# Optimization experiments

Hardware: AMD Instinct MI355X
Metric: run time of the kernel (lower is better)

The kernel has to match this reference:

```python
import jax, jax.numpy as jnp
from jax import lax
import numpy as np

SHAPE = (50, 60, 65)   # -> after net: (17, 27, 32), flatten = 14688
NEG = 0.01             # LeakyReLU default slope
B, N = 8, 80000        # batch size, total active voxels


def _lrelu(x):
    return jnp.where(x >= 0, x, NEG * x)


def _sparse_conv(x, w, b, m):
    # Regular (non-submanifold) sparse conv == dense VALID conv on densified
    # input (inactive sites are 0 so they contribute nothing). Output site is
    # active iff any input site in the kernel footprint is active; bias is
    # added only at active output sites.
    k = w.shape[2]
    y = lax.conv_general_dilated(x, w, (1, 1, 1), 'VALID',
                                 dimension_numbers=('NCDHW', 'OIDHW', 'NCDHW'))
    m2 = lax.reduce_window(m, 0.0, lax.max, (1, 1, k, k, k), (1, 1, 1, 1, 1), 'VALID')
    y = jnp.where(m2 > 0, y + b[None, :, None, None, None], 0.0)
    return y, m2


def _sparse_maxpool(x, m, k):
    # spconv SparseMaxPool: max over ACTIVE sites only (inactive excluded, not 0)
    xm = jnp.where(m > 0, x, -jnp.inf)
    p = lax.reduce_window(xm, -jnp.inf, lax.max, (1, 1, k, k, k), (1, 1, 1, 1, 1), 'VALID')
    m2 = lax.reduce_window(m, 0.0, lax.max, (1, 1, k, k, k), (1, 1, 1, 1, 1), 'VALID')
    return jnp.where(m2 > 0, p, 0.0), m2


def setup_inputs() -> dict:
    key = jax.random.key(0)
    ks = jax.random.split(key, 24)
    D, H, W = SHAPE
    features = jax.random.normal(ks[0], (N, 1), dtype=jnp.float32)
    bi = jax.random.randint(ks[1], (N,), 0, B)
    zi = jax.random.randint(ks[2], (N,), 0, D)
    yi = jax.random.randint(ks[3], (N,), 0, H)
    xi = jax.random.randint(ks[4], (N,), 0, W)
    coors = jnp.stack([bi, zi, yi, xi], axis=1).astype(jnp.int32)
    s = 0.05
    p = {}
    p['w1'] = jax.random.normal(ks[5], (32, 1, 4, 4, 4), jnp.float32) * s
    p['b1'] = jax.random.normal(ks[6], (32,), jnp.float32) * s
    p['w2'] = jax.random.normal(ks[7], (32, 32, 4, 4, 4), jnp.float32) * s
    p['b2'] = jax.random.normal(ks[8], (32,), jnp.float32) * s
    p['w3'] = jax.random.normal(ks[9], (32, 32, 4, 4, 4), jnp.float32) * s
    p['b3'] = jax.random.normal(ks[10], (32,), jnp.float32) * s
    p['w4'] = jax.random.normal(ks[11], (32, 32, 4, 4, 4), jnp.float32) * s
    p['b4'] = jax.random.normal(ks[12], (32,), jnp.float32) * s
    p['w5'] = jax.random.normal(ks[13], (32, 32, 4, 4, 4), jnp.float32) * s
    p['b5'] = jax.random.normal(ks[14], (32,), jnp.float32) * s
    p['w6'] = jax.random.normal(ks[15], (32, 32, 4, 4, 4), jnp.float32) * s
    p['b6'] = jax.random.normal(ks[16], (32,), jnp.float32) * s
    p['w7'] = jax.random.normal(ks[17], (1, 32, 4, 4, 4), jnp.float32) * s
    p['b7'] = jax.random.normal(ks[18], (1,), jnp.float32) * s
    p['W8'] = jax.random.normal(ks[19], (14688, 1000), jnp.float32) * 0.01
    p['b8'] = jax.random.normal(ks[20], (1000,), jnp.float32) * s
    p['W9'] = jax.random.normal(ks[21], (1000, 1000), jnp.float32) * 0.03
    p['b9'] = jax.random.normal(ks[22], (1000,), jnp.float32) * s
    p['W10'] = jax.random.normal(ks[23], (1000, 1), jnp.float32) * 0.03
    p['b10'] = jnp.zeros((1,), jnp.float32)
    return dict(features=features, coors=coors, batch_size=B, **p)


def reference(features, coors, batch_size,
              w1, b1, w2, b2, w3, b3, w4, b4, w5, b5, w6, b6, w7, b7,
              W8, b8, W9, b9, W10, b10):
    D, H, W = SHAPE
    bi, zi, yi, xi = coors[:, 0], coors[:, 1], coors[:, 2], coors[:, 3]
    dense = jnp.zeros((batch_size, 1, D, H, W), features.dtype)
    dense = dense.at[bi, 0, zi, yi, xi].set(features[:, 0])
    mask = jnp.zeros((batch_size, 1, D, H, W), features.dtype)
    mask = mask.at[bi, 0, zi, yi, xi].set(1.0)

    x, m = _sparse_conv(dense, w1, b1, mask); x = _lrelu(x)
    x, m = _sparse_conv(x, w2, b2, m);        x = _lrelu(x)
    x, m = _sparse_maxpool(x, m, 5)
    x, m = _sparse_conv(x, w3, b3, m);        x = _lrelu(x)
    x, m = _sparse_conv(x, w4, b4, m);        x = _lrelu(x)
    x, m = _sparse_maxpool(x, m, 5)
    x, m = _sparse_conv(x, w5, b5, m);        x = _lrelu(x)
    x, m = _sparse_conv(x, w6, b6, m);        x = _lrelu(x)
    x, m = _sparse_conv(x, w7, b7, m);        x = _lrelu(x)
    x, m = _sparse_maxpool(x, m, 5)

    # ToDense (inactive sites already 0) + Flatten -> [B, 14688]
    h = x.reshape(x.shape[0], -1)
    h = _lrelu(h @ W8 + b8)
    h = _lrelu(h @ W9 + b9)
    out = _lrelu(h @ W10 + b10)
    return out
```

## Files before the change

### kernel.cpp

```cpp
#include <hip/hip_runtime.h>
#include <cstddef>


#define NEGSLOPE 0.01f
#define NINF (-3.0e38f)

#define TZ 4
#define TY 4
#define TXT 16
#define IZ 7
#define IY 7
#define IX 19
#define NV (IZ*IY*IX)

typedef __attribute__((ext_vector_type(8)))  short    short8;
typedef __attribute__((ext_vector_type(4)))  unsigned uint4v;
typedef __attribute__((ext_vector_type(16))) float    floatx16;

__device__ __forceinline__ float lrelu(float v) { return v >= 0.f ? v : NEGSLOPE * v; }

__device__ __forceinline__ unsigned short f2bf(float f) {
  unsigned b = __float_as_uint(f);
  return (unsigned short)((b + 0x7fffu + ((b >> 16) & 1u)) >> 16);
}
__device__ __forceinline__ float bf2f(unsigned short h) {
  return __uint_as_float(((unsigned)h) << 16);
}
__device__ __forceinline__ unsigned splitpair(float a, float b, unsigned& lo) {
  unsigned short ha = f2bf(a), hb = f2bf(b);
  unsigned short la = f2bf(a - bf2f(ha)), lb = f2bf(b - bf2f(hb));
  lo = (unsigned)la | ((unsigned)lb << 16);
  return (unsigned)ha | ((unsigned)hb << 16);
}

__device__ __forceinline__ short8 ld_frag(const uint2* s2, int v, int oct) {
  uint2 u0 = s2[v * 5 + oct * 2];
  uint2 u1 = s2[v * 5 + oct * 2 + 1];
  uint4v t; t.x = u0.x; t.y = u0.y; t.z = u1.x; t.w = u1.y;
  return __builtin_bit_cast(short8, t);
}

__global__ void k_claim(const int* __restrict__ coors, unsigned* __restrict__ claim, int N) {
  int i = blockIdx.x * blockDim.x + threadIdx.x;
  if (i >= N) return;
  int b = coors[4*i], z = coors[4*i+1], y = coors[4*i+2], x = coors[4*i+3];
  int v = ((b*50 + z)*60 + y)*65 + x;
  atomicMax(&claim[v], (unsigned)(i + 1));
}

__global__ void k_scatter(const int* __restrict__ coors, const float* __restrict__ feat,
                          const unsigned* __restrict__ claim,
                          float* __restrict__ x0, float* __restrict__ m0, int N) {
  int i = blockIdx.x * blockDim.x + threadIdx.x;
  if (i >= N) return;
  int b = coors[4*i], z = coors[4*i+1], y = coors[4*i+2], x = coors[4*i+3];
  int v = ((b*50 + z)*60 + y)*65 + x;
  m0[v] = 1.f;
  if (claim[v] == (unsigned)(i + 1)) x0[v] = feat[i];
}

__global__ void k_repack(const float* __restrict__ w, float* __restrict__ wr, int CI, int CO) {
  int i = blockIdx.x * blockDim.x + threadIdx.x;
  int tot = CO * CI * 64;
  if (i >= tot) return;
  int k = i & 63;
  int ci = (i >> 6) % CI;
  int co = i / (64 * CI);
  wr[(k * CI + ci) * CO + co] = w[i];
}

__global__ void k_repack_mfma(const float* __restrict__ w, unsigned short* __restrict__ tbl) {
  int i = blockIdx.x * blockDim.x + threadIdx.x;
  if (i >= 64*4*2*64) return;
  int lane = i & 63; int t = i >> 6;
  int pack = t & 1; t >>= 1;
  int pass = t & 3; int tap = t >> 2;
  int co = lane & 31; int oct = lane >> 5;
#pragma unroll
  for (int j = 0; j < 8; ++j) {
    int k = oct * 8 + j;
    int ci = pass * 8 + (k & 7);
    int part = ((k >> 3) ^ pack) & 1;
    float wv = w[((co * 32 + ci) << 6) + tap];
    unsigned short wh = f2bf(wv);
    unsigned short r = part ? f2bf(wv - bf2f(wh)) : wh;
    tbl[(size_t)i * 8 + j] = r;
  }
}

__global__ void kd_z(const float* __restrict__ in, float* __restrict__ o,
                     int Zi, int Yi, int Xi, int Zo, int K, int nI) {
  int gid = blockIdx.x * blockDim.x + threadIdx.x;
  int perOut = Zo * Yi * Xi;
  if (gid >= nI * perOut) return;
  int item = gid / perOut;
  int r = gid - item * perOut;
  int x = r % Xi; int t = r / Xi;
  int y = t % Yi; int z = t / Yi;
  const float* ib = in + (size_t)item * Zi * Yi * Xi;
  float mx = 0.f;
  for (int d = 0; d < K; d++) mx = fmaxf(mx, ib[((z + d) * Yi + y) * Xi + x]);
  o[gid] = mx;
}

__global__ void kd_y(const float* __restrict__ in, float* __restrict__ o,
                     int Zo, int Yi, int Xi, int Yo, int K, int nI) {
  int gid = blockIdx.x * blockDim.x + threadIdx.x;
  int perOut = Zo * Yo * Xi;
  if (gid >= nI * perOut) return;
  int item = gid / perOut;
  int r = gid - item * perOut;
  int x = r % Xi; int t = r / Xi;
  int y = t % Yo; int z = t / Yo;
  const float* ib = in + (size_t)item * Zo * Yi * Xi;
  float mx = 0.f;
  for (int d = 0; d < K; d++) mx = fmaxf(mx, ib[(z * Yi + y + d) * Xi + x]);
  o[gid] = mx;
}

__global__ void kd_x(const float* __restrict__ in, float* __restrict__ o,
                     int Zo, int Yo, int Xi, int Xo, int K, int nI) {
  int gid = blockIdx.x * blockDim.x + threadIdx.x;
  int perOut = Zo * Yo * Xo;
  if (gid >= nI * perOut) return;
  int item = gid / perOut;
  int r = gid - item * perOut;
  int x = r % Xo; int t = r / Xo;
  int y = t % Yo; int z = t / Yo;
  const float* ib = in + (size_t)item * Zo * Yo * Xi;
  float mx = 0.f;
  for (int d = 0; d < K; d++) mx = fmaxf(mx, ib[(z * Yo + y) * Xi + x + d]);
  o[gid] = mx;
}

__global__ __launch_bounds__(256, 4)
void k_conv32m(const float* __restrict__ in, const unsigned short* __restrict__ tbl,
               const float* __restrict__ bias, const float* __restrict__ mo,
               float* __restrict__ out, int splitOut,
               int Zi, int Yi, int Xi, int Zo, int Yo, int Xo,
               int tilesZ, int tilesY, int tilesX) {
  __shared__ unsigned sU[NV * 10];
  const int perIn = Zi * Yi * Xi;
  const int perOut = Zo * Yo * Xo;
  int bid = blockIdx.x;
  int txi = bid % tilesX; bid /= tilesX;
  int tyi = bid % tilesY; bid /= tilesY;
  int tzi = bid % tilesZ; int item = bid / tilesZ;
  const int z0 = tzi * TZ, y0 = tyi * TY, x0 = txi * TXT;
  const int tid = threadIdx.x;
  const int lane = tid & 63;
  const int col = lane & 31;
  const int oct = lane >> 5;
  const int wv  = tid >> 6;

  int lvBase0, lvBase1;
  {
    int vt0 = (2*wv + 0)*32 + col;
    int vt1 = (2*wv + 1)*32 + col;
    lvBase0 = ((vt0 >> 6)*IY + ((vt0 >> 4) & 3))*IX + (vt0 & 15);
    lvBase1 = ((vt1 >> 6)*IY + ((vt1 >> 4) & 3))*IX + (vt1 & 15);
  }

  floatx16 acc0, acc1;
#pragma unroll
  for (int r = 0; r < 16; ++r) { acc0[r] = 0.f; acc1[r] = 0.f; }

  const char* inB = (const char*)in + (size_t)item * perIn * 128;
  const char* tb = (const char*)tbl + lane * 16;
  uint2* s2 = (uint2*)sU;

  const char* gptr[4];
  int lidx[4];
#pragma unroll
  for (int it = 0; it < 4; ++it) {
    int idx = tid + it * 256;
    gptr[it] = nullptr; lidx[it] = -1;
    if (idx < NV) {
      int iz = idx / (IY * IX); int r = idx - iz * (IY * IX);
      int iy = r / IX; int ix = r - iy * IX;
      int gz = z0 + iz, gy = y0 + iy, gx = x0 + ix;
      lidx[it] = idx * 5;
      if (gz < Zi && gy < Yi && gx < Xi)
        gptr[it] = inB + (size_t)((gz * Yi + gy) * Xi + gx) * 128;
    }
  }

  uint4 hreg[4], lreg[4];
  const uint4 zz = make_uint4(0u, 0u, 0u, 0u);
#pragma unroll
  for (int it = 0; it < 4; ++it) {
    hreg[it] = zz; lreg[it] = zz;
    if (gptr[it]) {
      hreg[it] = *(const uint4*)(gptr[it]);
      lreg[it] = *(const uint4*)(gptr[it] + 16);
    }
  }

#pragma unroll 1
  for (int p = 0; p < 4; ++p) {
    __syncthreads();
#pragma unroll
    for (int it = 0; it < 4; ++it) {
      if (lidx[it] >= 0) {
        s2[lidx[it] + 0] = make_uint2(hreg[it].x, hreg[it].y);
        s2[lidx[it] + 1] = make_uint2(hreg[it].z, hreg[it].w);
        s2[lidx[it] + 2] = make_uint2(lreg[it].x, lreg[it].y);
        s2[lidx[it] + 3] = make_uint2(lreg[it].z, lreg[it].w);
      }
    }
    __syncthreads();
    if (p < 3) {
      int po = (p + 1) * 32;
#pragma unroll
      for (int it = 0; it < 4; ++it) {
        hreg[it] = zz; lreg[it] = zz;
        if (gptr[it]) {
          hreg[it] = *(const uint4*)(gptr[it] + po);
          lreg[it] = *(const uint4*)(gptr[it] + po + 16);
        }
      }
    }

    const char* tp = tb + (size_t)p * 2048;
#pragma unroll 2
    for (int tap = 0; tap < 64; ++tap) {
      int kz = tap >> 4, ky = (tap >> 2) & 3, kx = tap & 3;
      int sOff = (kz * IY + ky) * IX + kx;
      short8 b0 = *(const short8*)(tp + (size_t)tap * 8192);
      short8 b1 = *(const short8*)(tp + (size_t)tap * 8192 + 1024);
      short8 a0 = ld_frag(s2, lvBase0 + sOff, oct);
      short8 a1 = ld_frag(s2, lvBase1 + sOff, oct);
      acc0 = __builtin_amdgcn_mfma_f32_32x32x16_bf16(a0, b0, acc0, 0, 0, 0);
      acc0 = __builtin_amdgcn_mfma_f32_32x32x16_bf16(a0, b1, acc0, 0, 0, 0);
      acc1 = __builtin_amdgcn_mfma_f32_32x32x16_bf16(a1, b0, acc1, 0, 0, 0);
      acc1 = __builtin_amdgcn_mfma_f32_32x32x16_bf16(a1, b1, acc1, 0, 0, 0);
    }
  }

  const float bco = bias[col];
#pragma unroll
  for (int gg = 0; gg < 2; ++gg) {
    int vtb = (2*wv + gg) * 32;
#pragma unroll
    for (int rg = 0; rg < 16; ++rg) {
      int row = (rg & 3) + 8 * (rg >> 2) + 4 * oct;
      int vt = vtb + row;
      int oz = vt >> 6, oy = (vt >> 4) & 3, ox = vt & 15;
      int gz = z0 + oz, gy = y0 + oy, gx = x0 + ox;
      if (gz < Zo && gy < Yo && gx < Xo) {
        int ov = item * perOut + (gz * Yo + gy) * Xo + gx;
        float val = (gg == 0) ? acc0[rg] : acc1[rg];
        bool act = mo[ov] > 0.f;
        float vv = lrelu(act ? (val + bco) : 0.f);
        if (!splitOut) {
          out[(size_t)ov * 32 + col] = vv;
        } else {
          unsigned short hs = f2bf(vv);
          unsigned short ls = f2bf(vv - bf2f(hs));
          char* op = (char*)out + (size_t)ov * 128 + ((col >> 3) << 5) + ((col & 7) << 1);
          *(unsigned short*)op = hs;
          *(unsigned short*)(op + 16) = ls;
        }
      }
    }
  }
}

__global__ __launch_bounds__(256, 2)
void k_conv1t(const float* __restrict__ in, const float* __restrict__ wr,
              const float* __restrict__ bias, const float* __restrict__ mo,
              float* __restrict__ out,
              int Zi, int Yi, int Xi, int Zo, int Yo, int Xo,
              int tilesZ, int tilesY, int tilesX) {
  __shared__ float sinf[NV];
  __shared__ float4 wsh[512];
  {
    const float4* wr4 = (const float4*)wr;
    for (int idx = threadIdx.x; idx < 512; idx += 256) wsh[idx] = wr4[idx];
  }
  const int perIn = Zi * Yi * Xi;
  const int perOut = Zo * Yo * Xo;
  int bid = blockIdx.x;
  int txi = bid % tilesX; bid /= tilesX;
  int tyi = bid % tilesY; bid /= tilesY;
  int tzi = bid % tilesZ; int item = bid / tilesZ;
  const int z0 = tzi * TZ, y0 = tyi * TY, x0 = txi * TXT;
  const int tid = threadIdx.x;
  const int ox = tid & 15, oy = (tid >> 4) & 3, oz = tid >> 6;

  const float* inb = in + (size_t)item * perIn;
  for (int idx = tid; idx < NV; idx += 256) {
    int iz = idx / (IY * IX); int r = idx - iz * (IY * IX);
    int iy = r / IX; int ix = r - iy * IX;
    int gz = z0 + iz, gy = y0 + iy, gx = x0 + ix;
    float val = 0.f;
    if (gz < Zi && gy < Yi && gx < Xi)
      val = inb[(size_t)((gz * Yi + gy) * Xi + gx)];
    sinf[idx] = val;
  }
  __syncthreads();

  float4 acc[8];
#pragma unroll
  for (int j = 0; j < 8; ++j) acc[j] = make_float4(0.f, 0.f, 0.f, 0.f);

#pragma unroll 1
  for (int tap = 0; tap < 64; ++tap) {
    int kz = tap >> 4, ky = (tap >> 2) & 3, kx = tap & 3;
    int lv = ((oz + kz) * IY + (oy + ky)) * IX + (ox + kx);
    float av = sinf[lv];
#pragma unroll
    for (int j = 0; j < 8; ++j) {
      float4 wvv = wsh[tap * 8 + j];
      acc[j].x = fmaf(av, wvv.x, acc[j].x);
      acc[j].y = fmaf(av, wvv.y, acc[j].y);
      acc[j].z = fmaf(av, wvv.z, acc[j].z);
      acc[j].w = fmaf(av, wvv.w, acc[j].w);
    }
  }

  int gz = z0 + oz, gy = y0 + oy, gx = x0 + ox;
  if (gz < Zo && gy < Yo && gx < Xo) {
    int ov = item * perOut + (gz * Yo + gy) * Xo + gx;
    bool act = mo[ov] > 0.f;
    const float4* b4 = (const float4*)bias;
    char* op = (char*)out + (size_t)ov * 128;
#pragma unroll
    for (int pp = 0; pp < 4; ++pp) {
      float4 r0 = acc[pp * 2], r1 = acc[pp * 2 + 1];
      float4 b0 = b4[pp * 2], b1 = b4[pp * 2 + 1];
      float v0 = lrelu(act ? (r0.x + b0.x) : 0.f);
      float v1 = lrelu(act ? (r0.y + b0.y) : 0.f);
      float v2 = lrelu(act ? (r0.z + b0.z) : 0.f);
      float v3 = lrelu(act ? (r0.w + b0.w) : 0.f);
      float v4 = lrelu(act ? (r1.x + b1.x) : 0.f);
      float v5 = lrelu(act ? (r1.y + b1.y) : 0.f);
      float v6 = lrelu(act ? (r1.z + b1.z) : 0.f);
      float v7 = lrelu(act ? (r1.w + b1.w) : 0.f);
      unsigned L0, L1, L2, L3;
      unsigned H0 = splitpair(v0, v1, L0);
      unsigned H1 = splitpair(v2, v3, L1);
      unsigned H2 = splitpair(v4, v5, L2);
      unsigned H3 = splitpair(v6, v7, L3);
      *(uint4*)(op + pp * 32)      = make_uint4(H0, H1, H2, H3);
      *(uint4*)(op + pp * 32 + 16) = make_uint4(L0, L1, L2, L3);
    }
  }
}

__global__ __launch_bounds__(256, 2)
void k_conv7t(const float* __restrict__ in, const float* __restrict__ wr,
              const float* __restrict__ bias, const float* __restrict__ mo,
              float* __restrict__ out,
              int Zi, int Yi, int Xi, int Zo, int Yo, int Xo,
              int tilesZ, int tilesY, int tilesX) {
  __shared__ float4 sin4[4][NV];
  __shared__ float4 wsh[512];
  {
    const float4* wr4 = (const float4*)wr;
    for (int idx = threadIdx.x; idx < 512; idx += 256) wsh[idx] = wr4[idx];
  }
  const int perIn = Zi * Yi * Xi;
  const int perOut = Zo * Yo * Xo;
  int bid = blockIdx.x;
  int txi = bid % tilesX; bid /= tilesX;
  int tyi = bid % tilesY; bid /= tilesY;
  int tzi = bid % tilesZ; int item = bid / tilesZ;
  const int z0 = tzi * TZ, y0 = tyi * TY, x0 = txi * TXT;
  const int tid = threadIdx.x;
  const int ox = tid & 15, oy = (tid >> 4) & 3, oz = tid >> 6;

  const float* inb = in + (size_t)item * perIn * 32;
  float acc = 0.f;

#pragma unroll 1
  for (int h = 0; h < 2; ++h) {
    __syncthreads();
    for (int idx = tid; idx < NV * 4; idx += 256) {
      int q = idx / NV; int v = idx - q * NV;
      int iz = v / (IY * IX); int r = v - iz * (IY * IX);
      int iy = r / IX; int ix = r - iy * IX;
      int gz = z0 + iz, gy = y0 + iy, gx = x0 + ix;
      float4 val = make_float4(0.f, 0.f, 0.f, 0.f);
      if (gz < Zi && gy < Yi && gx < Xi)
        val = *(const float4*)(inb + (size_t)((gz * Yi + gy) * Xi + gx) * 32 + h * 16 + q * 4);
      sin4[q][v] = val;
    }
    __syncthreads();
#pragma unroll 1
    for (int tap = 0; tap < 64; ++tap) {
      int kz = tap >> 4, ky = (tap >> 2) & 3, kx = tap & 3;
      int lv = ((oz + kz) * IY + (oy + ky)) * IX + (ox + kx);
      float4 a0 = sin4[0][lv];
      float4 a1 = sin4[1][lv];
      float4 a2 = sin4[2][lv];
      float4 a3 = sin4[3][lv];
      float4 w0 = wsh[tap * 8 + h * 4 + 0];
      float4 w1 = wsh[tap * 8 + h * 4 + 1];
      float4 w2 = wsh[tap * 8 + h * 4 + 2];
      float4 w3 = wsh[tap * 8 + h * 4 + 3];
      acc += a0.x*w0.x + a0.y*w0.y + a0.z*w0.z + a0.w*w0.w
           + a1.x*w1.x + a1.y*w1.y + a1.z*w1.z + a1.w*w1.w
           + a2.x*w2.x + a2.y*w2.y + a2.z*w2.z + a2.w*w2.w
           + a3.x*w3.x + a3.y*w3.y + a3.z*w3.z + a3.w*w3.w;
    }
  }

  int gz = z0 + oz, gy = y0 + oy, gx = x0 + ox;
  if (gz < Zo && gy < Yo && gx < Xo) {
    int ov = item * perOut + (gz * Yo + gy) * Xo + gx;
    bool act = mo[ov] > 0.f;
    out[ov] = lrelu(act ? (acc + bias[0]) : 0.f);
  }
}

__global__ void k_pool_z(const float* __restrict__ in, const float* __restrict__ m,
                         float* __restrict__ out, int Zi, int Yi, int Xi, int Zo, int nI) {
  int gid = blockIdx.x * blockDim.x + threadIdx.x;
  int perOut = Zo * Yi * Xi;
  int tot = nI * perOut * 8;
  if (gid >= tot) return;
  int c4 = gid & 7; int v = gid >> 3;
  int item = v / perOut;
  int r = v - item * perOut;
  int x = r % Xi; int t = r / Xi;
  int y = t % Yi; int z = t / Yi;
  int ib = item * Zi * Yi * Xi;
  float4 acc = {NINF, NINF, NINF, NINF};
  for (int j = 0; j < 5; j++) {
    int vi = ib + ((z + j)*Yi + y)*Xi + x;
    if (m[vi] > 0.f) {
      float4 val = *(const float4*)(in + (size_t)vi*32 + c4*4);
      acc.x = fmaxf(acc.x, val.x); acc.y = fmaxf(acc.y, val.y);
      acc.z = fmaxf(acc.z, val.z); acc.w = fmaxf(acc.w, val.w);
    }
  }
  *(float4*)(out + (size_t)v*32 + c4*4) = acc;
}

__global__ void k_pool_y(const float* __restrict__ in, float* __restrict__ out,
                         int Z, int Yi, int Xi, int Yo, int nI) {
  int gid = blockIdx.x * blockDim.x + threadIdx.x;
  int perOut = Z * Yo * Xi;
  int tot = nI * perOut * 8;
  if (gid >= tot) return;
  int c4 = gid & 7; int v = gid >> 3;
  int item = v / perOut;
  int r = v - item * perOut;
  int x = r % Xi; int t = r / Xi;
  int y = t % Yo; int z = t / Yo;
  int ib = item * Z * Yi * Xi;
  float4 acc = {NINF, NINF, NINF, NINF};
  for (int j = 0; j < 5; j++) {
    int vi = ib + (z*Yi + y + j)*Xi + x;
    float4 val = *(const float4*)(in + (size_t)vi*32 + c4*4);
    acc.x = fmaxf(acc.x, val.x); acc.y = fmaxf(acc.y, val.y);
    acc.z = fmaxf(acc.z, val.z); acc.w = fmaxf(acc.w, val.w);
  }
  *(float4*)(out + (size_t)v*32 + c4*4) = acc;
}

__global__ void k_pool_x(const float* __restrict__ in, const float* __restrict__ mp,
                         float* __restrict__ out, int Z, int Y, int Xi, int Xo, int nI) {
  int gid = blockIdx.x * blockDim.x + threadIdx.x;
  int perOut = Z * Y * Xo;
  int tot = nI * perOut * 8;
  if (gid >= tot) return;
  int c4 = gid & 7; int v = gid >> 3;
  int item = v / perOut;
  int r = v - item * perOut;
  int x = r % Xo; int t = r / Xo;
  int y = t % Y; int z = t / Y;
  int ib = item * Z * Y * Xi;
  float4 acc = {NINF, NINF, NINF, NINF};
  for (int j = 0; j < 5; j++) {
    int vi = ib + (z*Y + y)*Xi + x + j;
    float4 val = *(const float4*)(in + (size_t)vi*32 + c4*4);
    acc.x = fmaxf(acc.x, val.x); acc.y = fmaxf(acc.y, val.y);
    acc.z = fmaxf(acc.z, val.z); acc.w = fmaxf(acc.w, val.w);
  }
  bool act = mp[v] > 0.f;
  float4 rr;
  rr.x = act ? acc.x : 0.f; rr.y = act ? acc.y : 0.f;
  rr.z = act ? acc.z : 0.f; rr.w = act ? acc.w : 0.f;
  unsigned lo01, lo23;
  unsigned h01 = splitpair(rr.x, rr.y, lo01);
  unsigned h23 = splitpair(rr.z, rr.w, lo23);
  char* op = (char*)out + (size_t)v * 128 + ((c4 >> 1) << 5) + ((c4 & 1) << 3);
  *(uint2*)op        = make_uint2(h01, h23);
  *(uint2*)(op + 16) = make_uint2(lo01, lo23);
}

__global__ void k_pool3(const float* __restrict__ xin, const float* __restrict__ m,
                        const float* __restrict__ mp, float* __restrict__ out, int nI) {
  int gid = blockIdx.x * blockDim.x + threadIdx.x;
  int perOut = 17 * 27 * 32;
  int tot = nI * perOut;
  if (gid >= tot) return;
  int item = gid / perOut;
  int r = gid - item * perOut;
  int x = r & 31; int t = r >> 5;
  int y = t % 27; int z = t / 27;
  const float* xb = xin + (size_t)item * 23436;
  const float* mb = m + (size_t)item * 23436;
  float acc = NINF;
  for (int dz = 0; dz < 5; dz++)
    for (int dy = 0; dy < 5; dy++) {
      const float* rowx = xb + (size_t)(((z + dz)*31 + y + dy)*36 + x);
      const float* rowm = mb + (size_t)(((z + dz)*31 + y + dy)*36 + x);
      for (int dx = 0; dx < 5; dx++)
        if (rowm[dx] > 0.f) acc = fmaxf(acc, rowx[dx]);
    }
  out[gid] = (mp[gid] > 0.f) ? acc : 0.f;
}

__global__ __launch_bounds__(256, 4)
void k_fc_part(const float* __restrict__ X, const float* __restrict__ Wm,
               float* __restrict__ part, int K, int Ncol, int Kc) {
  __shared__ float sm[16][16][8];
  int ks = blockIdx.y;
  int k0 = ks * Kc;
  int k1 = k0 + Kc; if (k1 > K) k1 = K;
  int cl = threadIdx.x & 15;
  int kt = threadIdx.x >> 4;
  int col = blockIdx.x * 16 + cl;
  float a0=0.f,a1=0.f,a2=0.f,a3=0.f,a4=0.f,a5=0.f,a6=0.f,a7=0.f;
  if (col < Ncol) {
    for (int k = k0 + kt; k < k1; k += 16) {
      float w = Wm[(size_t)k * Ncol + col];
      a0 += X[0 * K + k] * w; a1 += X[1 * K + k] * w;
      a2 += X[2 * K + k] * w; a3 += X[3 * K + k] * w;
      a4 += X[4 * K + k] * w; a5 += X[5 * K + k] * w;
      a6 += X[6 * K + k] * w; a7 += X[7 * K + k] * w;
    }
  }
  sm[kt][cl][0]=a0; sm[kt][cl][1]=a1; sm[kt][cl][2]=a2; sm[kt][cl][3]=a3;
  sm[kt][cl][4]=a4; sm[kt][cl][5]=a5; sm[kt][cl][6]=a6; sm[kt][cl][7]=a7;
  __syncthreads();
  if (threadIdx.x < 128) {
    int c = threadIdx.x & 15;
    int b = threadIdx.x >> 4;
    float s = 0.f;
#pragma unroll
    for (int k = 0; k < 16; k++) s += sm[k][c][b];
    int cc = blockIdx.x * 16 + c;
    if (cc < Ncol) part[((size_t)ks * 8 + b) * Ncol + cc] = s;
  }
}

__global__ void k_fc_fin(const float* __restrict__ part, int ns,
                         const float* __restrict__ bias, float* __restrict__ out, int Ncol) {
  int i = blockIdx.x * blockDim.x + threadIdx.x;
  if (i >= 8 * Ncol) return;
  int b = i / Ncol;
  int c = i - b * Ncol;
  float s = 0.f;
  for (int ks = 0; ks < ns; ks++) s += part[((size_t)ks * 8 + b) * Ncol + c];
  out[i] = lrelu(s + bias[c]);
}

__global__ __launch_bounds__(256, 4)
void k_fc(const float* __restrict__ X, const float* __restrict__ Wm,
          const float* __restrict__ bias, float* __restrict__ out,
          int K, int Ncol) {
  __shared__ float sm[16][16][8];
  int cl = threadIdx.x & 15;
  int kt = threadIdx.x >> 4;
  int col = blockIdx.x * 16 + cl;
  float a0=0.f,a1=0.f,a2=0.f,a3=0.f,a4=0.f,a5=0.f,a6=0.f,a7=0.f;
  if (col < Ncol) {
    for (int k = kt; k < K; k += 16) {
      float w = Wm[(size_t)k * Ncol + col];
      a0 += X[0 * K + k] * w; a1 += X[1 * K + k] * w;
      a2 += X[2 * K + k] * w; a3 += X[3 * K + k] * w;
      a4 += X[4 * K + k] * w; a5 += X[5 * K + k] * w;
      a6 += X[6 * K + k] * w; a7 += X[7 * K + k] * w;
    }
  }
  sm[kt][cl][0]=a0; sm[kt][cl][1]=a1; sm[kt][cl][2]=a2; sm[kt][cl][3]=a3;
  sm[kt][cl][4]=a4; sm[kt][cl][5]=a5; sm[kt][cl][6]=a6; sm[kt][cl][7]=a7;
  __syncthreads();
  if (threadIdx.x < 128) {
    int c = threadIdx.x & 15;
    int b = threadIdx.x >> 4;
    float s = 0.f;
#pragma unroll
    for (int k = 0; k < 16; k++) s += sm[k][c][b];
    int cc = blockIdx.x * 16 + c;
    if (cc < Ncol) out[b * Ncol + cc] = lrelu(s + bias[cc]);
  }
}

static inline int G256(long long n) { return (int)((n + 255) / 256); }

extern "C" void kernel_launch(void* const* d_in, const int* in_sizes, int n_in,
                              void* d_out, int out_size, void* d_ws, size_t ws_size,
                              hipStream_t stream) {
  const float* feat  = (const float*)d_in[0];
  const int*   coors = (const int*)d_in[1];
  const float* w1 = (const float*)d_in[3];  const float* b1 = (const float*)d_in[4];
  const float* w2 = (const float*)d_in[5];  const float* b2 = (const float*)d_in[6];
  const float* w3 = (const float*)d_in[7];  const float* b3 = (const float*)d_in[8];
  const float* w4 = (const float*)d_in[9];  const float* b4 = (const float*)d_in[10];
  const float* w5 = (const float*)d_in[11]; const float* b5 = (const float*)d_in[12];
  const float* w6 = (const float*)d_in[13]; const float* b6 = (const float*)d_in[14];
  const float* w7 = (const float*)d_in[15]; const float* b7 = (const float*)d_in[16];
  const float* W8 = (const float*)d_in[17]; const float* b8 = (const float*)d_in[18];
  const float* W9 = (const float*)d_in[19]; const float* b9 = (const float*)d_in[20];
  const float* W10= (const float*)d_in[21]; const float* b10= (const float*)d_in[22];
  float* out = (float*)d_out;

  char* ws = (char*)d_ws;
  size_t off = 0;
  auto alloc = [&](size_t nfloats) -> float* {
    float* p = (float*)(ws + off);
    off += ((nfloats * 4 + 1023) / 1024) * 1024;
    return p;
  };

  float* x0  = alloc(1560000);
  float* m0  = alloc(1560000);
  float* m1  = alloc(8 * 166098);
  float* m2  = alloc(8 * 140184);
  float* mp1 = alloc(8 * 110000);
  float* m3  = alloc(8 * 90428);
  float* m4  = alloc(8 * 73304);
  float* mp2 = alloc(8 * 54000);
  float* m5  = alloc(8 * 41958);
  float* m6  = alloc(8 * 31824);
  float* m7  = alloc(8 * 23436);
  float* mp3 = alloc(8 * 14688);
  float* p3  = alloc(8 * 14688);
  float* dt1 = alloc(8 * 183300);
  float* dt2 = alloc(8 * 174135);
  float* wr1 = alloc(2048);
  float* wr7 = alloc(2048);
  unsigned short* tb2 = (unsigned short*)alloc(131072);
  unsigned short* tb3 = (unsigned short*)alloc(131072);
  unsigned short* tb4 = (unsigned short*)alloc(131072);
  unsigned short* tb5 = (unsigned short*)alloc(131072);
  unsigned short* tb6 = (unsigned short*)alloc(131072);
  float* part= alloc(64000);
  float* h8  = alloc(8000);
  float* h9  = alloc(8000);
  size_t fixedOff = off;

  const size_t perItemAB = ((size_t)5315136*4 + 1023)/1024*1024
                         + ((size_t)4485888*4 + 1023)/1024*1024
                         + ((size_t)23436*4 + 1023)/1024*1024;
  int G = 0;
  for (int g : {8, 4, 2, 1})
    if (fixedOff + (size_t)g * perItemAB <= ws_size) { G = g; break; }
  if (G == 0) return;

  float* A  = alloc((size_t)G * 5315136);
  float* Bb = alloc((size_t)G * 4485888);
  float* x7 = alloc((size_t)G * 23436);
  unsigned* claim = (unsigned*)A;

  hipMemsetAsync(claim, 0, 1560000 * 4, stream);
  hipMemsetAsync(x0,    0, 1560000 * 4, stream);
  hipMemsetAsync(m0,    0, 1560000 * 4, stream);

  k_repack<<<G256(32*1*64),  256, 0, stream>>>(w1, wr1, 1, 32);
  k_repack<<<G256(1*32*64),  256, 0, stream>>>(w7, wr7, 32, 1);
  k_repack_mfma<<<128, 256, 0, stream>>>(w2, tb2);
  k_repack_mfma<<<128, 256, 0, stream>>>(w3, tb3);
  k_repack_mfma<<<128, 256, 0, stream>>>(w4, tb4);
  k_repack_mfma<<<128, 256, 0, stream>>>(w5, tb5);
  k_repack_mfma<<<128, 256, 0, stream>>>(w6, tb6);

  const int N = 80000;
  k_claim  <<<G256(N), 256, 0, stream>>>(coors, claim, N);
  k_scatter<<<G256(N), 256, 0, stream>>>(coors, feat, claim, x0, m0, N);

  auto dil3 = [&](const float* src, float* dst,
                  int Zi, int Yi, int Xi, int Zo, int Yo, int Xo, int K) {
    kd_z<<<G256((long long)8*Zo*Yi*Xi), 256, 0, stream>>>(src, dt1, Zi,Yi,Xi, Zo, K, 8);
    kd_y<<<G256((long long)8*Zo*Yo*Xi), 256, 0, stream>>>(dt1, dt2, Zo,Yi,Xi, Yo, K, 8);
    kd_x<<<G256((long long)8*Zo*Yo*Xo), 256, 0, stream>>>(dt2, dst, Zo,Yo,Xi, Xo, K, 8);
  };
  dil3(m0,  m1,  50,60,65, 47,57,62, 4);
  dil3(m1,  m2,  47,57,62, 44,54,59, 4);
  dil3(m2,  mp1, 44,54,59, 40,50,55, 5);
  dil3(mp1, m3,  40,50,55, 37,47,52, 4);
  dil3(m3,  m4,  37,47,52, 34,44,49, 4);
  dil3(m4,  mp2, 34,44,49, 30,40,45, 5);
  dil3(mp2, m5,  30,40,45, 27,37,42, 4);
  dil3(m5,  m6,  27,37,42, 24,34,39, 4);
  dil3(m6,  m7,  24,34,39, 21,31,36, 4);
  dil3(m7,  mp3, 21,31,36, 17,27,32, 5);

  auto conv32 = [&](const float* in, const unsigned short* tbl, const float* bias,
                    const float* mo, float* o, int splitOut,
                    int Zi, int Yi, int Xi, int Zo, int Yo, int Xo, int nI) {
    int tz = (Zo + TZ - 1) / TZ, ty = (Yo + TY - 1) / TY, tx = (Xo + TXT - 1) / TXT;
    k_conv32m<<<nI * tz * ty * tx, 256, 0, stream>>>(
        in, tbl, bias, mo, o, splitOut, Zi, Yi, Xi, Zo, Yo, Xo, tz, ty, tx);
  };

  for (int g0 = 0; g0 < 8; g0 += G) {
    const float* x0g  = x0  + (size_t)g0 * 195000;
    const float* m1g  = m1  + (size_t)g0 * 166098;
    const float* m2g  = m2  + (size_t)g0 * 140184;
    const float* mp1g = mp1 + (size_t)g0 * 110000;
    const float* m3g  = m3  + (size_t)g0 * 90428;
    const float* m4g  = m4  + (size_t)g0 * 73304;
    const float* mp2g = mp2 + (size_t)g0 * 54000;
    const float* m5g  = m5  + (size_t)g0 * 41958;
    const float* m6g  = m6  + (size_t)g0 * 31824;
    const float* m7g  = m7  + (size_t)g0 * 23436;
    const float* mp3g = mp3 + (size_t)g0 * 14688;

    {
      int tz = (47 + TZ - 1) / TZ, ty = (57 + TY - 1) / TY, tx = (62 + TXT - 1) / TXT;
      k_conv1t<<<G * tz * ty * tx, 256, 0, stream>>>(
          x0g, wr1, b1, m1g, A, 50,60,65, 47,57,62, tz, ty, tx);
    }
    conv32(A, tb2, b2, m2g, Bb, 0, 47,57,62, 44,54,59, G);
    k_pool_z<<<G256((long long)G*127440*8), 256, 0, stream>>>(Bb, m2g,  A,  44,54,59, 40, G);
    k_pool_y<<<G256((long long)G*118000*8), 256, 0, stream>>>(A,  Bb, 40,54,59, 50, G);
    k_pool_x<<<G256((long long)G*110000*8), 256, 0, stream>>>(Bb, mp1g, A,  40,50,59, 55, G);
    conv32(A, tb3, b3, m3g, Bb, 1, 40,50,55, 37,47,52, G);
    conv32(Bb, tb4, b4, m4g, A, 0, 37,47,52, 34,44,49, G);
    k_pool_z<<<G256((long long)G*64680*8), 256, 0, stream>>>(A,  m4g,  Bb, 34,44,49, 30, G);
    k_pool_y<<<G256((long long)G*58800*8), 256, 0, stream>>>(Bb, A,  30,44,49, 40, G);
    k_pool_x<<<G256((long long)G*54000*8), 256, 0, stream>>>(A,  mp2g, Bb, 30,40,49, 45, G);
    conv32(Bb, tb5, b5, m5g, A, 1, 30,40,45, 27,37,42, G);
    conv32(A, tb6, b6, m6g, Bb, 0, 27,37,42, 24,34,39, G);
    {
      int tz = (21 + TZ - 1) / TZ, ty = (31 + TY - 1) / TY, tx = (36 + TXT - 1) / TXT;
      k_conv7t<<<G * tz * ty * tx, 256, 0, stream>>>(
          Bb, wr7, b7, m7g, x7, 24,34,39, 21,31,36, tz, ty, tx);
    }
    k_pool3<<<G256((long long)G*14688), 256, 0, stream>>>(
        x7, m7g, mp3g, p3 + (size_t)g0 * 14688, G);
  }

  k_fc_part<<<dim3(63, 8), 256, 0, stream>>>(p3, W8, part, 14688, 1000, 1836);
  k_fc_fin <<<G256(8000), 256, 0, stream>>>(part, 8, b8, h8, 1000);
  k_fc_part<<<dim3(63, 4), 256, 0, stream>>>(h8, W9, part, 1000, 1000, 250);
  k_fc_fin <<<G256(8000), 256, 0, stream>>>(part, 4, b9, h9, 1000);
  k_fc<<<1, 256, 0, stream>>>(h9, W10, b10, out, 1000, 1);
}
```

Measured before the change: 3.431 ms.

## Double conv output tile in Y so each wave reuses weight fragments across four accumulators

Grows the 32-channel conv block tile from 4x4x16 to 4x8x16 output voxels. Each wave now owns four 32-row accumulator groups instead of two, so every weight fragment loaded from global memory feeds four MFMA pairs, and the halo overhead per output voxel shrinks. The cost is a larger LDS footprint, more staging registers (6 slots per thread), twice the accumulator registers, and launch bounds lowered to 2 blocks per CU. More edge tiles are also partially wasted on small late-stage volumes.

Result: faster. 3.361 ms (-2.0%).

```diff
diff --git a/kernel.cpp b/kernel.cpp
--- a/kernel.cpp
+++ b/kernel.cpp
@@ -12,6 +12,15 @@
 #define IY 7
 #define IX 19
 #define NV (IZ*IY*IX)
+
+#define MTZ 4
+#define MTY 8
+#define MTXT 16
+#define MIZ 7
+#define MIY 11
+#define MIX 19
+#define MNV (MIZ*MIY*MIX)
+#define MST 6
 
 typedef __attribute__((ext_vector_type(8)))  short    short8;
 typedef __attribute__((ext_vector_type(4)))  unsigned uint4v;
@@ -133,51 +142,55 @@
   o[gid] = mx;
 }
 
-__global__ __launch_bounds__(256, 4)
+__global__ __launch_bounds__(256, 2)
 void k_conv32m(const float* __restrict__ in, const unsigned short* __restrict__ tbl,
                const float* __restrict__ bias, const float* __restrict__ mo,
                float* __restrict__ out, int splitOut,
                int Zi, int Yi, int Xi, int Zo, int Yo, int Xo,
                int tilesZ, int tilesY, int tilesX) {
-  __shared__ unsigned sU[NV * 10];
+  __shared__ unsigned sU[MNV * 10];
   const int perIn = Zi * Yi * Xi;
   const int perOut = Zo * Yo * Xo;
   int bid = blockIdx.x;
   int txi = bid % tilesX; bid /= tilesX;
   int tyi = bid % tilesY; bid /= tilesY;
   int tzi = bid % tilesZ; int item = bid / tilesZ;
-  const int z0 = tzi * TZ, y0 = tyi * TY, x0 = txi * TXT;
+  const int z0 = tzi * MTZ, y0 = tyi * MTY, x0 = txi * MTXT;
   const int tid = threadIdx.x;
   const int lane = tid & 63;
   const int col = lane & 31;
   const int oct = lane >> 5;
   const int wv  = tid >> 6;
 
-  int lvBase0, lvBase1;
+  int lvB0, lvB1, lvB2, lvB3;
   {
-    int vt0 = (2*wv + 0)*32 + col;
-    int vt1 = (2*wv + 1)*32 + col;
-    lvBase0 = ((vt0 >> 6)*IY + ((vt0 >> 4) & 3))*IX + (vt0 & 15);
-    lvBase1 = ((vt1 >> 6)*IY + ((vt1 >> 4) & 3))*IX + (vt1 & 15);
-  }
-
-  floatx16 acc0, acc1;
-#pragma unroll
-  for (int r = 0; r < 16; ++r) { acc0[r] = 0.f; acc1[r] = 0.f; }
+    int vt0 = (4*wv + 0)*32 + col;
+    int vt1 = (4*wv + 1)*32 + col;
+    int vt2 = (4*wv + 2)*32 + col;
+    int vt3 = (4*wv + 3)*32 + col;
+    lvB0 = ((vt0 >> 7)*MIY + ((vt0 >> 4) & 7))*MIX + (vt0 & 15);
+    lvB1 = ((vt1 >> 7)*MIY + ((vt1 >> 4) & 7))*MIX + (vt1 & 15);
+    lvB2 = ((vt2 >> 7)*MIY + ((vt2 >> 4) & 7))*MIX + (vt2 & 15);
+    lvB3 = ((vt3 >> 7)*MIY + ((vt3 >> 4) & 7))*MIX + (vt3 & 15);
+  }
+
+  floatx16 acc0, acc1, acc2, acc3;
+#pragma unroll
+  for (int r = 0; r < 16; ++r) { acc0[r] = 0.f; acc1[r] = 0.f; acc2[r] = 0.f; acc3[r] = 0.f; }
 
   const char* inB = (const char*)in + (size_t)item * perIn * 128;
   const char* tb = (const char*)tbl + lane * 16;
   uint2* s2 = (uint2*)sU;
 
-  const char* gptr[4];
-  int lidx[4];
-#pragma unroll
-  for (int it = 0; it < 4; ++it) {
+  const char* gptr[MST];
+  int lidx[MST];
+#pragma unroll
+  for (int it = 0; it < MST; ++it) {
     int idx = tid + it * 256;
     gptr[it] = nullptr; lidx[it] = -1;
-    if (idx < NV) {
-      int iz = idx / (IY * IX); int r = idx - iz * (IY * IX);
-      int iy = r / IX; int ix = r - iy * IX;
+    if (idx < MNV) {
+      int iz = idx / (MIY * MIX); int r = idx - iz * (MIY * MIX);
+      int iy = r / MIX; int ix = r - iy * MIX;
       int gz = z0 + iz, gy = y0 + iy, gx = x0 + ix;
       lidx[it] = idx * 5;
       if (gz < Zi && gy < Yi && gx < Xi)
@@ -185,10 +198,10 @@
     }
   }
 
-  uint4 hreg[4], lreg[4];
+  uint4 hreg[MST], lreg[MST];
   const uint4 zz = make_uint4(0u, 0u, 0u, 0u);
 #pragma unroll
-  for (int it = 0; it < 4; ++it) {
+  for (int it = 0; it < MST; ++it) {
     hreg[it] = zz; lreg[it] = zz;
     if (gptr[it]) {
       hreg[it] = *(const uint4*)(gptr[it]);
@@ -200,7 +213,7 @@
   for (int p = 0; p < 4; ++p) {
     __syncthreads();
 #pragma unroll
-    for (int it = 0; it < 4; ++it) {
+    for (int it = 0; it < MST; ++it) {
       if (lidx[it] >= 0) {
         s2[lidx[it] + 0] = make_uint2(hreg[it].x, hreg[it].y);
         s2[lidx[it] + 1] = make_uint2(hreg[it].z, hreg[it].w);
@@ -212,7 +225,7 @@
     if (p < 3) {
       int po = (p + 1) * 32;
 #pragma unroll
-      for (int it = 0; it < 4; ++it) {
+      for (int it = 0; it < MST; ++it) {
         hreg[it] = zz; lreg[it] = zz;
         if (gptr[it]) {
           hreg[it] = *(const uint4*)(gptr[it] + po);
@@ -225,31 +238,38 @@
 #pragma unroll 2
     for (int tap = 0; tap < 64; ++tap) {
       int kz = tap >> 4, ky = (tap >> 2) & 3, kx = tap & 3;
-      int sOff = (kz * IY + ky) * IX + kx;
+      int sOff = (kz * MIY + ky) * MIX + kx;
       short8 b0 = *(const short8*)(tp + (size_t)tap * 8192);
       short8 b1 = *(const short8*)(tp + (size_t)tap * 8192 + 1024);
-      short8 a0 = ld_frag(s2, lvBase0 + sOff, oct);
-      short8 a1 = ld_frag(s2, lvBase1 + sOff, oct);
+      short8 a0 = ld_frag(s2, lvB0 + sOff, oct);
+      short8 a1 = ld_frag(s2, lvB1 + sOff, oct);
+      short8 a2 = ld_frag(s2, lvB2 + sOff, oct);
+      short8 a3 = ld_frag(s2, lvB3 + sOff, oct);
       acc0 = __builtin_amdgcn_mfma_f32_32x32x16_bf16(a0, b0, acc0, 0, 0, 0);
       acc0 = __builtin_amdgcn_mfma_f32_32x32x16_bf16(a0, b1, acc0, 0, 0, 0);
       acc1 = __builtin_amdgcn_mfma_f32_32x32x16_bf16(a1, b0, acc1, 0, 0, 0);
       acc1 = __builtin_amdgcn_mfma_f32_32x32x16_bf16(a1, b1, acc1, 0, 0, 0);
+      acc2 = __builtin_amdgcn_mfma_f32_32x32x16_bf16(a2, b0, acc2, 0, 0, 0);
+      acc2 = __builtin_amdgcn_mfma_f32_32x32x16_bf16(a2, b1, acc2, 0, 0, 0);
+      acc3 = __builtin_amdgcn_mfma_f32_32x32x16_bf16(a3, b0, acc3, 0, 0, 0);
+      acc3 = __builtin_amdgcn_mfma_f32_32x32x16_bf16(a3, b1, acc3, 0, 0, 0);
     }
   }
 
   const float bco = bias[col];
 #pragma unroll
-  for (int gg = 0; gg < 2; ++gg) {
-    int vtb = (2*wv + gg) * 32;
+  for (int gg = 0; gg < 4; ++gg) {
+    int vtb = (4*wv + gg) * 32;
 #pragma unroll
     for (int rg = 0; rg < 16; ++rg) {
       int row = (rg & 3) + 8 * (rg >> 2) + 4 * oct;
       int vt = vtb + row;
-      int oz = vt >> 6, oy = (vt >> 4) & 3, ox = vt & 15;
+      int oz = vt >> 7, oy = (vt >> 4) & 7, ox = vt & 15;
       int gz = z0 + oz, gy = y0 + oy, gx = x0 + ox;
       if (gz < Zo && gy < Yo && gx < Xo) {
         int ov = item * perOut + (gz * Yo + gy) * Xo + gx;
-        float val = (gg == 0) ? acc0[rg] : acc1[rg];
+        float val = (gg == 0) ? acc0[rg] : (gg == 1) ? acc1[rg]
+                  : (gg == 2) ? acc2[rg] : acc3[rg];
         bool act = mo[ov] > 0.f;
         float vv = lrelu(act ? (val + bco) : 0.f);
         if (!splitOut) {
@@ -694,7 +714,7 @@
   auto conv32 = [&](const float* in, const unsigned short* tbl, const float* bias,
                     const float* mo, float* o, int splitOut,
                     int Zi, int Yi, int Xi, int Zo, int Yo, int Xo, int nI) {
-    int tz = (Zo + TZ - 1) / TZ, ty = (Yo + TY - 1) / TY, tx = (Xo + TXT - 1) / TXT;
+    int tz = (Zo + MTZ - 1) / MTZ, ty = (Yo + MTY - 1) / MTY, tx = (Xo + MTXT - 1) / MTXT;
     k_conv32m<<<nI * tz * ty * tx, 256, 0, stream>>>(
         in, tbl, bias, mo, o, splitOut, Zi, Yi, Xi, Zo, Yo, Xo, tz, ty, tx);
   };
```
